# Kernel optimization log

Measured on AMD Instinct MI355X. Metric: run time of the kernel, lower is better.

## Reference

```python
import jax, jax.numpy as jnp
import numpy as np

# Hardcoded in FixedActionDecoder.__init__:
# action_words = [[click,submit,target,focus],[select,text,noun,username,password],[copy],[paste]]
ACTION_INDEX = jnp.array([0, 0, 0, 0, 1, 1, 1, 1, 1, 2, 3], dtype=jnp.int32)
POINT_SIZE = 11
ACTION_SIZE = 4
EPS = 1e-8  # F.cosine_similarity default eps


def setup_inputs() -> dict:
    key = jax.random.key(0)
    k1, k2 = jax.random.split(key)
    B, D = 1_000_000, 64
    return {
        "embedded_words": jax.random.normal(k1, (B, D), dtype=jnp.float32),
        "action_vectors": jax.random.normal(k2, (D, POINT_SIZE), dtype=jnp.float32),
    }


def reference(embedded_words, action_vectors):
    # Cosine similarity along the embedding dim (torch clamps each norm to eps).
    x = embedded_words / jnp.maximum(
        jnp.linalg.norm(embedded_words, axis=1, keepdims=True), EPS)          # [B, D]
    a = action_vectors / jnp.maximum(
        jnp.linalg.norm(action_vectors, axis=0, keepdims=True), EPS)          # [D, P]
    sims = x @ a                                                              # [B, P]
    # global_max_pool over batch_action_index == per-batch segment-max over actions.
    seg = jax.ops.segment_max(sims.T, ACTION_INDEX,
                              num_segments=ACTION_SIZE).T                     # [B, A]
    action_idx = jnp.argmax(seg, axis=1)                                      # [B]
    # one-hot scatter: ret[action_idx] = 1.0
    return jax.nn.one_hot(action_idx, ACTION_SIZE, dtype=embedded_words.dtype)
```

## Files before the change

kernel.cpp:

```cpp
#include <hip/hip_runtime.h>


#define NP 11
#define TAU 1e-3f
#define LROW 36
#define NROWS 128

__device__ __align__(16) float g_W32[704];
__device__ double g_W64[704];
__device__ unsigned long long g_bits[1 << 20];

__global__ void prep(const float* __restrict__ A) {
    int p = threadIdx.x;
    if (p < NP) {
        double ss = 0.0;
        for (int d = 0; d < 64; ++d) { double v = (double)A[d * NP + p]; ss += v * v; }
        double sc = 1.0 / fmax(sqrt(ss), 1e-8);
        for (int d = 0; d < 64; ++d) {
            double w = (double)A[d * NP + p] * sc;
            g_W64[d * NP + p] = w;
            g_W32[(d >> 2) * 44 + (d & 3) * NP + p] = (float)w;
        }
    }
}

__device__ __forceinline__ void argmax_gap(const float* s, int& idx, float& gap) {
    float m0 = fmaxf(fmaxf(s[0], s[1]), fmaxf(s[2], s[3]));
    float m1 = fmaxf(fmaxf(fmaxf(s[4], s[5]), s[6]), fmaxf(s[7], s[8]));
    float m2 = s[9], m3 = s[10];
    idx = 0; float best = m0;
    if (m1 > best) { best = m1; idx = 1; }
    if (m2 > best) { best = m2; idx = 2; }
    if (m3 > best) { best = m3; idx = 3; }
    float second = -3.4e38f;
    if (idx != 0) second = fmaxf(second, m0);
    if (idx != 1) second = fmaxf(second, m1);
    if (idx != 2) second = fmaxf(second, m2);
    if (idx != 3) second = fmaxf(second, m3);
    gap = best - second;
}

__global__ __launch_bounds__(128) void decode_f32(const float* __restrict__ X,
                                                  float* __restrict__ out, int B) {
    __shared__ float xbuf[2][NROWS][LROW];
    __shared__ float w_lds[704];

    const int tid = threadIdx.x;
    const int lane = tid & 63;
    const int wv = tid >> 6;
    float(*buf)[LROW] = xbuf[wv];

    for (int t = tid; t < 176; t += 128)
        reinterpret_cast<float4*>(w_lds)[t] =
            reinterpret_cast<const float4*>(g_W32)[t];
    __syncthreads();

    const float4* X4 = reinterpret_cast<const float4*>(X);
    const int gwave = blockIdx.x * 2 + wv;
    const int nwaves = gridDim.x * 2;

    #pragma unroll 1
    for (int base = gwave * NROWS; base < B; base += nwaves * NROWS) {
        float acc0[NP], acc1[NP];
        #pragma unroll
        for (int p = 0; p < NP; ++p) { acc0[p] = 0.0f; acc1[p] = 0.0f; }

        #pragma unroll
        for (int st = 0; st < 2; ++st) {
            #pragma unroll
            for (int i = 0; i < 16; ++i) {
                int fid = i * 64 + lane;
                int row = fid >> 3;
                int f = fid & 7;
                int r = base + row;
                if (r >= B) r = B - 1;
                float4 v = X4[(size_t)r * 16 + st * 8 + f];
                *reinterpret_cast<float4*>(&buf[row][f * 4]) = v;
            }
            __builtin_amdgcn_wave_barrier();

            #pragma unroll 1
            for (int kk = 0; kk < 8; ++kk) {
                const float* wrow = &w_lds[(st * 8 + kk) * 44];
                float4 x0 = *reinterpret_cast<const float4*>(&buf[lane][kk * 4]);
                float4 x1 = *reinterpret_cast<const float4*>(&buf[lane + 64][kk * 4]);
                #pragma unroll
                for (int p = 0; p < NP; ++p) {
                    float w0 = wrow[0 * NP + p], w1 = wrow[1 * NP + p];
                    float w2 = wrow[2 * NP + p], w3 = wrow[3 * NP + p];
                    float t0 = fmaf(x0.x, w0, acc0[p]);
                    t0 = fmaf(x0.y, w1, t0);
                    t0 = fmaf(x0.z, w2, t0);
                    acc0[p] = fmaf(x0.w, w3, t0);
                    float t1 = fmaf(x1.x, w0, acc1[p]);
                    t1 = fmaf(x1.y, w1, t1);
                    t1 = fmaf(x1.z, w2, t1);
                    acc1[p] = fmaf(x1.w, w3, t1);
                }
            }
            __builtin_amdgcn_wave_barrier();
        }

        int idx0, idx1; float gap0, gap1;
        argmax_gap(acc0, idx0, gap0);
        argmax_gap(acc1, idx1, gap1);

        unsigned long long m0 = __ballot(gap0 < TAU);
        unsigned long long m1 = __ballot(gap1 < TAU);
        if (lane == 0) {
            g_bits[(base >> 6) + 0] = m0;
            g_bits[(base >> 6) + 1] = m1;
        }

        int r0 = base + lane, r1 = base + 64 + lane;
        if (r0 < B) {
            float4 o;
            o.x = (idx0 == 0) ? 1.0f : 0.0f;
            o.y = (idx0 == 1) ? 1.0f : 0.0f;
            o.z = (idx0 == 2) ? 1.0f : 0.0f;
            o.w = (idx0 == 3) ? 1.0f : 0.0f;
            reinterpret_cast<float4*>(out)[r0] = o;
        }
        if (r1 < B) {
            float4 o;
            o.x = (idx1 == 0) ? 1.0f : 0.0f;
            o.y = (idx1 == 1) ? 1.0f : 0.0f;
            o.z = (idx1 == 2) ? 1.0f : 0.0f;
            o.w = (idx1 == 3) ? 1.0f : 0.0f;
            reinterpret_cast<float4*>(out)[r1] = o;
        }
    }
}

__global__ __launch_bounds__(256) void repair(const float* __restrict__ X,
                                              float* __restrict__ out, int B) {
    const int nwords = (B + 63) >> 6;
    for (int t = blockIdx.x * blockDim.x + threadIdx.x; t < nwords;
         t += gridDim.x * blockDim.x) {
        unsigned long long m = g_bits[t];
        while (m) {
            int b = __builtin_ctzll(m);
            m &= m - 1;
            int row = t * 64 + b;
            if (row >= B) continue;

            double s[NP];
            #pragma unroll
            for (int p = 0; p < NP; ++p) s[p] = 0.0;
            #pragma unroll 1
            for (int d = 0; d < 64; ++d) {
                double x = (double)X[(size_t)row * 64 + d];
                #pragma unroll
                for (int p = 0; p < NP; ++p)
                    s[p] = fma(x, g_W64[d * NP + p], s[p]);
            }

            double m0 = fmax(fmax(s[0], s[1]), fmax(s[2], s[3]));
            double m1 = fmax(fmax(fmax(s[4], s[5]), s[6]), fmax(s[7], s[8]));
            double m2 = s[9], m3 = s[10];
            int idx = 0; double best = m0;
            if (m1 > best) { best = m1; idx = 1; }
            if (m2 > best) { best = m2; idx = 2; }
            if (m3 > best) { best = m3; idx = 3; }

            float4 o;
            o.x = (idx == 0) ? 1.0f : 0.0f;
            o.y = (idx == 1) ? 1.0f : 0.0f;
            o.z = (idx == 2) ? 1.0f : 0.0f;
            o.w = (idx == 3) ? 1.0f : 0.0f;
            reinterpret_cast<float4*>(out)[row] = o;
        }
    }
}

extern "C" void kernel_launch(void* const* d_in, const int* in_sizes, int n_in,
                              void* d_out, int out_size, void* d_ws, size_t ws_size,
                              hipStream_t stream) {
    const float* X = (const float*)d_in[0];
    const float* A = (const float*)d_in[1];
    float* out = (float*)d_out;
    const int B = in_sizes[0] / 64;

    hipLaunchKernelGGL(prep, dim3(1), dim3(64), 0, stream, A);
    hipLaunchKernelGGL(decode_f32, dim3(1024), dim3(128), 0, stream, X, out, B);
    hipLaunchKernelGGL(repair, dim3(128), dim3(256), 0, stream, X, out, B);
}
```

Measured before the change: 88.64 us.

## Prefetch X tiles directly into LDS with double-buffered async global_load_lds

Each wave now streams its rows with global_load_lds straight into a swizzled LDS buffer for each half of the row, which skips the register staging step. The next tile's loads are issued right after the current half is consumed, so memory fetch overlaps with compute, and hand-placed vmcnt waits order the pipeline. Weights now live in the workspace and are read from global or constant memory instead of being staged in LDS, and the grid is halved to 512 blocks. This relies on fragile inline waitcnt counts and sched barriers. Per-wave LDS use also rises, which may limit occupancy.

Result: slower. 99.58 us (+12.3%).

```diff
diff --git a/kernel.cpp b/kernel.cpp
--- a/kernel.cpp
+++ b/kernel.cpp
@@ -3,14 +3,12 @@
 
 #define NP 11
 #define TAU 1e-3f
-#define LROW 36
-#define NROWS 128
-
-__device__ __align__(16) float g_W32[704];
-__device__ double g_W64[704];
+
 __device__ unsigned long long g_bits[1 << 20];
 
-__global__ void prep(const float* __restrict__ A) {
+__global__ void prep(const float* __restrict__ A, void* __restrict__ ws) {
+    float* W32 = (float*)ws;
+    double* W64 = (double*)((char*)ws + 4096);
     int p = threadIdx.x;
     if (p < NP) {
         double ss = 0.0;
@@ -18,11 +16,47 @@
         double sc = 1.0 / fmax(sqrt(ss), 1e-8);
         for (int d = 0; d < 64; ++d) {
             double w = (double)A[d * NP + p] * sc;
-            g_W64[d * NP + p] = w;
-            g_W32[(d >> 2) * 44 + (d & 3) * NP + p] = (float)w;
-        }
-    }
-}
+            W64[d * NP + p] = w;
+            W32[(d >> 2) * 44 + (d & 3) * NP + p] = (float)w;
+        }
+    }
+}
+
+#define ISSUE(tbase, phase, ldsbuf)                                            \
+    {                                                                          \
+        _Pragma("unroll") for (int i = 0; i < 16; ++i) {                       \
+            int row_local = i * 8 + (lane >> 3);                               \
+            int r = (tbase) + row_local;                                       \
+            if (r >= B) r = B - 1;     \
+            const float4* src = X4 + (size_t)r * 16 + (phase) * 8 + fsrc;      \
+            __builtin_amdgcn_global_load_lds(                                  \
+                (const __attribute__((address_space(1))) void*)src,            \
+                (__attribute__((address_space(3))) void*)((ldsbuf) + i * 64),  \
+                16, 0, 0);                                                     \
+        }                                                                      \
+    }
+
+#define COMPUTE(phase, buf)                                                    \
+    {                                                                          \
+        _Pragma("unroll 1") for (int kk = 0; kk < 8; ++kk) {                   \
+            const int sw = kk ^ s7;                                            \
+            float4 x0 = (buf)[lane * 8 + sw];                                  \
+            float4 x1 = (buf)[(lane + 64) * 8 + sw];                           \
+            const float* wrow = W + ((phase) * 8 + kk) * 44;                   \
+            _Pragma("unroll") for (int p = 0; p < NP; ++p) {                   \
+                float w0 = wrow[p], w1 = wrow[NP + p];                         \
+                float w2 = wrow[2 * NP + p], w3 = wrow[3 * NP + p];            \
+                float t0 = fmaf(x0.x, w0, acc0[p]);                            \
+                t0 = fmaf(x0.y, w1, t0);                                       \
+                t0 = fmaf(x0.z, w2, t0);                                       \
+                acc0[p] = fmaf(x0.w, w3, t0);                                  \
+                float t1 = fmaf(x1.x, w0, acc1[p]);                            \
+                t1 = fmaf(x1.y, w1, t1);                                       \
+                t1 = fmaf(x1.z, w2, t1);                                       \
+                acc1[p] = fmaf(x1.w, w3, t1);                                  \
+            }                                                                  \
+        }                                                                      \
+    }
 
 __device__ __forceinline__ void argmax_gap(const float* s, int& idx, float& gap) {
     float m0 = fmaxf(fmaxf(s[0], s[1]), fmaxf(s[2], s[3]));
@@ -40,66 +74,51 @@
     gap = best - second;
 }
 
-__global__ __launch_bounds__(128) void decode_f32(const float* __restrict__ X,
-                                                  float* __restrict__ out, int B) {
-    __shared__ float xbuf[2][NROWS][LROW];
-    __shared__ float w_lds[704];
+__global__ __launch_bounds__(128) void decode(const float* __restrict__ X,
+                                              float* __restrict__ out,
+                                              const float* __restrict__ W,
+                                              int B) {
+    __shared__ float4 sbuf[2][2][1024];
 
     const int tid = threadIdx.x;
     const int lane = tid & 63;
     const int wv = tid >> 6;
-    float(*buf)[LROW] = xbuf[wv];
-
-    for (int t = tid; t < 176; t += 128)
-        reinterpret_cast<float4*>(w_lds)[t] =
-            reinterpret_cast<const float4*>(g_W32)[t];
-    __syncthreads();
+    const int s7 = lane & 7;
+    const int fsrc = s7 ^ (lane >> 3);
+    float4* buf0 = &sbuf[wv][0][0];
+    float4* buf1 = &sbuf[wv][1][0];
 
     const float4* X4 = reinterpret_cast<const float4*>(X);
     const int gwave = blockIdx.x * 2 + wv;
-    const int nwaves = gridDim.x * 2;
+    const int stride = gridDim.x * 2 * 128;
+    const int base0 = gwave * 128;
+    if (base0 >= B) return;
+
+    ISSUE(base0, 0, buf0);
+    ISSUE(base0, 1, buf1);
 
     #pragma unroll 1
-    for (int base = gwave * NROWS; base < B; base += nwaves * NROWS) {
+    for (int base = base0; base < B; base += stride) {
+        const int next = base + stride;
+        const bool pf = next < B;
+
         float acc0[NP], acc1[NP];
         #pragma unroll
         for (int p = 0; p < NP; ++p) { acc0[p] = 0.0f; acc1[p] = 0.0f; }
 
-        #pragma unroll
-        for (int st = 0; st < 2; ++st) {
-            #pragma unroll
-            for (int i = 0; i < 16; ++i) {
-                int fid = i * 64 + lane;
-                int row = fid >> 3;
-                int f = fid & 7;
-                int r = base + row;
-                if (r >= B) r = B - 1;
-                float4 v = X4[(size_t)r * 16 + st * 8 + f];
-                *reinterpret_cast<float4*>(&buf[row][f * 4]) = v;
-            }
-            __builtin_amdgcn_wave_barrier();
-
-            #pragma unroll 1
-            for (int kk = 0; kk < 8; ++kk) {
-                const float* wrow = &w_lds[(st * 8 + kk) * 44];
-                float4 x0 = *reinterpret_cast<const float4*>(&buf[lane][kk * 4]);
-                float4 x1 = *reinterpret_cast<const float4*>(&buf[lane + 64][kk * 4]);
-                #pragma unroll
-                for (int p = 0; p < NP; ++p) {
-                    float w0 = wrow[0 * NP + p], w1 = wrow[1 * NP + p];
-                    float w2 = wrow[2 * NP + p], w3 = wrow[3 * NP + p];
-                    float t0 = fmaf(x0.x, w0, acc0[p]);
-                    t0 = fmaf(x0.y, w1, t0);
-                    t0 = fmaf(x0.z, w2, t0);
-                    acc0[p] = fmaf(x0.w, w3, t0);
-                    float t1 = fmaf(x1.x, w0, acc1[p]);
-                    t1 = fmaf(x1.y, w1, t1);
-                    t1 = fmaf(x1.z, w2, t1);
-                    acc1[p] = fmaf(x1.w, w3, t1);
-                }
-            }
-            __builtin_amdgcn_wave_barrier();
-        }
+        asm volatile("s_waitcnt vmcnt(16)" ::: "memory");
+        __builtin_amdgcn_sched_barrier(0);
+        COMPUTE(0, buf0);
+        if (pf) ISSUE(next, 0, buf0);
+
+        if (pf) {
+            asm volatile("s_waitcnt vmcnt(16)" ::: "memory");
+        } else {
+            asm volatile("s_waitcnt vmcnt(0)" ::: "memory");
+        }
+        __builtin_amdgcn_sched_barrier(0);
+        COMPUTE(1, buf1);
+        if (pf) ISSUE(next, 1, buf1);
 
         int idx0, idx1; float gap0, gap1;
         argmax_gap(acc0, idx0, gap0);
@@ -133,7 +152,10 @@
 }
 
 __global__ __launch_bounds__(256) void repair(const float* __restrict__ X,
-                                              float* __restrict__ out, int B) {
+                                              float* __restrict__ out,
+                                              const void* __restrict__ ws,
+                                              int B) {
+    const double* W64 = (const double*)((const char*)ws + 4096);
     const int nwords = (B + 63) >> 6;
     for (int t = blockIdx.x * blockDim.x + threadIdx.x; t < nwords;
          t += gridDim.x * blockDim.x) {
@@ -152,7 +174,7 @@
                 double x = (double)X[(size_t)row * 64 + d];
                 #pragma unroll
                 for (int p = 0; p < NP; ++p)
-                    s[p] = fma(x, g_W64[d * NP + p], s[p]);
+                    s[p] = fma(x, W64[d * NP + p], s[p]);
             }
 
             double m0 = fmax(fmax(s[0], s[1]), fmax(s[2], s[3]));
@@ -181,7 +203,8 @@
     float* out = (float*)d_out;
     const int B = in_sizes[0] / 64;
 
-    hipLaunchKernelGGL(prep, dim3(1), dim3(64), 0, stream, A);
-    hipLaunchKernelGGL(decode_f32, dim3(1024), dim3(128), 0, stream, X, out, B);
-    hipLaunchKernelGGL(repair, dim3(128), dim3(256), 0, stream, X, out, B);
-}
+    hipLaunchKernelGGL(prep, dim3(1), dim3(64), 0, stream, A, d_ws);
+    hipLaunchKernelGGL(decode, dim3(512), dim3(128), 0, stream,
+                       X, out, (const float*)d_ws, B);
+    hipLaunchKernelGGL(repair, dim3(128), dim3(256), 0, stream, X, out, d_ws, B);
+}
```

## Software-pipeline X loads through registers with 256-row wave tiles

Applied to the files above, without the earlier changes.

Each wave now handles 256 rows, split into four 16-float column quarters. The next quarter's global loads are issued into registers while the current quarter is computed out of LDS, so global memory latency overlaps with the FMA work. Each lane holds four rows of accumulators, which raises register pressure. The grid shrinks to 768 blocks and the LDS row pitch drops to 20 floats, which can change bank conflicts.

Result: slower. 201.0 us (+126.8%).

```diff
diff --git a/kernel.cpp b/kernel.cpp
--- a/kernel.cpp
+++ b/kernel.cpp
@@ -3,8 +3,7 @@
 
 #define NP 11
 #define TAU 1e-3f
-#define LROW 36
-#define NROWS 128
+#define QS 20
 
 __device__ __align__(16) float g_W32[704];
 __device__ double g_W64[704];
@@ -40,15 +39,15 @@
     gap = best - second;
 }
 
-__global__ __launch_bounds__(128) void decode_f32(const float* __restrict__ X,
-                                                  float* __restrict__ out, int B) {
-    __shared__ float xbuf[2][NROWS][LROW];
+__global__ __launch_bounds__(128) void decode(const float* __restrict__ X,
+                                              float* __restrict__ out, int B) {
+    __shared__ float xq[2][256][QS];
     __shared__ float w_lds[704];
 
     const int tid = threadIdx.x;
     const int lane = tid & 63;
     const int wv = tid >> 6;
-    float(*buf)[LROW] = xbuf[wv];
+    float(*buf)[QS] = xq[wv];
 
     for (int t = tid; t < 176; t += 128)
         reinterpret_cast<float4*>(w_lds)[t] =
@@ -57,77 +56,93 @@
 
     const float4* X4 = reinterpret_cast<const float4*>(X);
     const int gwave = blockIdx.x * 2 + wv;
-    const int nwaves = gridDim.x * 2;
+    const int stride = gridDim.x * 2 * 256;
+    const int base0 = gwave * 256;
+    if (base0 >= B) return;
+
+    const int srow = lane >> 2;
+    const int sf = lane & 3;
+
+    float4 st[16];
+
+    #pragma unroll
+    for (int i = 0; i < 16; ++i) {
+        int r = base0 + i * 16 + srow;
+        if (r >= B) r = B - 1;
+        st[i] = X4[(size_t)r * 16 + sf];
+    }
 
     #pragma unroll 1
-    for (int base = gwave * NROWS; base < B; base += nwaves * NROWS) {
-        float acc0[NP], acc1[NP];
+    for (int base = base0; base < B; base += stride) {
+        const int next = base + stride;
+
+        float acc[4][NP];
         #pragma unroll
-        for (int p = 0; p < NP; ++p) { acc0[p] = 0.0f; acc1[p] = 0.0f; }
-
-        #pragma unroll
-        for (int st = 0; st < 2; ++st) {
+        for (int j = 0; j < 4; ++j)
             #pragma unroll
-            for (int i = 0; i < 16; ++i) {
-                int fid = i * 64 + lane;
-                int row = fid >> 3;
-                int f = fid & 7;
-                int r = base + row;
-                if (r >= B) r = B - 1;
-                float4 v = X4[(size_t)r * 16 + st * 8 + f];
-                *reinterpret_cast<float4*>(&buf[row][f * 4]) = v;
-            }
+            for (int p = 0; p < NP; ++p) acc[j][p] = 0.0f;
+
+        #pragma unroll 1
+        for (int q = 0; q < 4; ++q) {
+            asm volatile("s_waitcnt vmcnt(0)" ::: "memory");
+            __builtin_amdgcn_sched_barrier(0);
+            #pragma unroll
+            for (int i = 0; i < 16; ++i)
+                *reinterpret_cast<float4*>(&buf[i * 16 + srow][sf * 4]) = st[i];
             __builtin_amdgcn_wave_barrier();
+            __builtin_amdgcn_sched_barrier(0);
+
+            int nq = q + 1, nbase = base;
+            if (nq == 4) { nq = 0; nbase = next; }
+            if (nbase < B) {
+                #pragma unroll
+                for (int i = 0; i < 16; ++i) {
+                    int r = nbase + i * 16 + srow;
+                    if (r >= B) r = B - 1;
+                    st[i] = X4[(size_t)r * 16 + nq * 4 + sf];
+                }
+            }
 
             #pragma unroll 1
-            for (int kk = 0; kk < 8; ++kk) {
-                const float* wrow = &w_lds[(st * 8 + kk) * 44];
+            for (int kk = 0; kk < 4; ++kk) {
+                const float* wrow = &w_lds[(q * 4 + kk) * 44];
                 float4 x0 = *reinterpret_cast<const float4*>(&buf[lane][kk * 4]);
                 float4 x1 = *reinterpret_cast<const float4*>(&buf[lane + 64][kk * 4]);
+                float4 x2 = *reinterpret_cast<const float4*>(&buf[lane + 128][kk * 4]);
+                float4 x3 = *reinterpret_cast<const float4*>(&buf[lane + 192][kk * 4]);
                 #pragma unroll
                 for (int p = 0; p < NP; ++p) {
-                    float w0 = wrow[0 * NP + p], w1 = wrow[1 * NP + p];
+                    float w0 = wrow[p], w1 = wrow[NP + p];
                     float w2 = wrow[2 * NP + p], w3 = wrow[3 * NP + p];
-                    float t0 = fmaf(x0.x, w0, acc0[p]);
-                    t0 = fmaf(x0.y, w1, t0);
-                    t0 = fmaf(x0.z, w2, t0);
-                    acc0[p] = fmaf(x0.w, w3, t0);
-                    float t1 = fmaf(x1.x, w0, acc1[p]);
-                    t1 = fmaf(x1.y, w1, t1);
-                    t1 = fmaf(x1.z, w2, t1);
-                    acc1[p] = fmaf(x1.w, w3, t1);
+                    float t;
+                    t = fmaf(x0.x, w0, acc[0][p]); t = fmaf(x0.y, w1, t);
+                    t = fmaf(x0.z, w2, t);         acc[0][p] = fmaf(x0.w, w3, t);
+                    t = fmaf(x1.x, w0, acc[1][p]); t = fmaf(x1.y, w1, t);
+                    t = fmaf(x1.z, w2, t);         acc[1][p] = fmaf(x1.w, w3, t);
+                    t = fmaf(x2.x, w0, acc[2][p]); t = fmaf(x2.y, w1, t);
+                    t = fmaf(x2.z, w2, t);         acc[2][p] = fmaf(x2.w, w3, t);
+                    t = fmaf(x3.x, w0, acc[3][p]); t = fmaf(x3.y, w1, t);
+                    t = fmaf(x3.z, w2, t);         acc[3][p] = fmaf(x3.w, w3, t);
                 }
             }
             __builtin_amdgcn_wave_barrier();
         }
 
-        int idx0, idx1; float gap0, gap1;
-        argmax_gap(acc0, idx0, gap0);
-        argmax_gap(acc1, idx1, gap1);
-
-        unsigned long long m0 = __ballot(gap0 < TAU);
-        unsigned long long m1 = __ballot(gap1 < TAU);
-        if (lane == 0) {
-            g_bits[(base >> 6) + 0] = m0;
-            g_bits[(base >> 6) + 1] = m1;
-        }
-
-        int r0 = base + lane, r1 = base + 64 + lane;
-        if (r0 < B) {
-            float4 o;
-            o.x = (idx0 == 0) ? 1.0f : 0.0f;
-            o.y = (idx0 == 1) ? 1.0f : 0.0f;
-            o.z = (idx0 == 2) ? 1.0f : 0.0f;
-            o.w = (idx0 == 3) ? 1.0f : 0.0f;
-            reinterpret_cast<float4*>(out)[r0] = o;
-        }
-        if (r1 < B) {
-            float4 o;
-            o.x = (idx1 == 0) ? 1.0f : 0.0f;
-            o.y = (idx1 == 1) ? 1.0f : 0.0f;
-            o.z = (idx1 == 2) ? 1.0f : 0.0f;
-            o.w = (idx1 == 3) ? 1.0f : 0.0f;
-            reinterpret_cast<float4*>(out)[r1] = o;
+        #pragma unroll
+        for (int j = 0; j < 4; ++j) {
+            int idx; float gap;
+            argmax_gap(acc[j], idx, gap);
+            unsigned long long m = __ballot(gap < TAU);
+            if (lane == 0) g_bits[(base >> 6) + j] = m;
+            int r = base + j * 64 + lane;
+            if (r < B) {
+                float4 o;
+                o.x = (idx == 0) ? 1.0f : 0.0f;
+                o.y = (idx == 1) ? 1.0f : 0.0f;
+                o.z = (idx == 2) ? 1.0f : 0.0f;
+                o.w = (idx == 3) ? 1.0f : 0.0f;
+                reinterpret_cast<float4*>(out)[r] = o;
+            }
         }
     }
 }
@@ -182,6 +197,6 @@
     const int B = in_sizes[0] / 64;
 
     hipLaunchKernelGGL(prep, dim3(1), dim3(64), 0, stream, A);
-    hipLaunchKernelGGL(decode_f32, dim3(1024), dim3(128), 0, stream, X, out, B);
+    hipLaunchKernelGGL(decode, dim3(768), dim3(128), 0, stream, X, out, B);
     hipLaunchKernelGGL(repair, dim3(128), dim3(256), 0, stream, X, out, B);
 }
```

## Transpose weight layout for float4 LDS loads, parallelize prep, cache weights in repair

Applied to the files above, without the earlier changes.

The normalized weight table is now stored so that the four k-values for each action point sit next to each other. The decode inner loop can then fetch them with one float4 LDS read instead of four scalar reads. The prep kernel now uses all 64 threads, with a shared-memory reduction, instead of 11 serial threads. The repair kernel stages the double-precision weights in LDS rather than reading global memory on every FMA. The aim is to cut LDS instruction count in the hot loop and to shorten the serial prep and repair phases.

Result: faster. 78.28 us (median of 3 runs) (-11.7%).

```diff
diff --git a/kernel.cpp b/kernel.cpp
--- a/kernel.cpp
+++ b/kernel.cpp
@@ -4,23 +4,34 @@
 #define NP 11
 #define TAU 1e-3f
 #define LROW 36
-#define NROWS 128
 
 __device__ __align__(16) float g_W32[704];
 __device__ double g_W64[704];
 __device__ unsigned long long g_bits[1 << 20];
 
 __global__ void prep(const float* __restrict__ A) {
-    int p = threadIdx.x;
-    if (p < NP) {
+    __shared__ double sq[64][NP + 1];
+    __shared__ double sc[NP];
+    const int d = threadIdx.x;
+    double a[NP];
+    #pragma unroll
+    for (int p = 0; p < NP; ++p) {
+        a[p] = (double)A[d * NP + p];
+        sq[d][p] = a[p] * a[p];
+    }
+    __syncthreads();
+    if (d < NP) {
         double ss = 0.0;
-        for (int d = 0; d < 64; ++d) { double v = (double)A[d * NP + p]; ss += v * v; }
-        double sc = 1.0 / fmax(sqrt(ss), 1e-8);
-        for (int d = 0; d < 64; ++d) {
-            double w = (double)A[d * NP + p] * sc;
-            g_W64[d * NP + p] = w;
-            g_W32[(d >> 2) * 44 + (d & 3) * NP + p] = (float)w;
-        }
+        #pragma unroll
+        for (int r = 0; r < 64; ++r) ss += sq[r][d];
+        sc[d] = 1.0 / fmax(sqrt(ss), 1e-8);
+    }
+    __syncthreads();
+    #pragma unroll
+    for (int p = 0; p < NP; ++p) {
+        double w = a[p] * sc[p];
+        g_W64[d * NP + p] = w;
+        g_W32[(d >> 2) * 44 + p * 4 + (d & 3)] = (float)w;
     }
 }
 
@@ -40,9 +51,9 @@
     gap = best - second;
 }
 
-__global__ __launch_bounds__(128) void decode_f32(const float* __restrict__ X,
-                                                  float* __restrict__ out, int B) {
-    __shared__ float xbuf[2][NROWS][LROW];
+__global__ __launch_bounds__(128) void decode(const float* __restrict__ X,
+                                              float* __restrict__ out, int B) {
+    __shared__ float xbuf[2][128][LROW];
     __shared__ float w_lds[704];
 
     const int tid = threadIdx.x;
@@ -60,7 +71,7 @@
     const int nwaves = gridDim.x * 2;
 
     #pragma unroll 1
-    for (int base = gwave * NROWS; base < B; base += nwaves * NROWS) {
+    for (int base = gwave * 128; base < B; base += nwaves * 128) {
         float acc0[NP], acc1[NP];
         #pragma unroll
         for (int p = 0; p < NP; ++p) { acc0[p] = 0.0f; acc1[p] = 0.0f; }
@@ -86,16 +97,15 @@
                 float4 x1 = *reinterpret_cast<const float4*>(&buf[lane + 64][kk * 4]);
                 #pragma unroll
                 for (int p = 0; p < NP; ++p) {
-                    float w0 = wrow[0 * NP + p], w1 = wrow[1 * NP + p];
-                    float w2 = wrow[2 * NP + p], w3 = wrow[3 * NP + p];
-                    float t0 = fmaf(x0.x, w0, acc0[p]);
-                    t0 = fmaf(x0.y, w1, t0);
-                    t0 = fmaf(x0.z, w2, t0);
-                    acc0[p] = fmaf(x0.w, w3, t0);
-                    float t1 = fmaf(x1.x, w0, acc1[p]);
-                    t1 = fmaf(x1.y, w1, t1);
-                    t1 = fmaf(x1.z, w2, t1);
-                    acc1[p] = fmaf(x1.w, w3, t1);
+                    float4 wq = *reinterpret_cast<const float4*>(&wrow[p * 4]);
+                    float t0 = fmaf(x0.x, wq.x, acc0[p]);
+                    t0 = fmaf(x0.y, wq.y, t0);
+                    t0 = fmaf(x0.z, wq.z, t0);
+                    acc0[p] = fmaf(x0.w, wq.w, t0);
+                    float t1 = fmaf(x1.x, wq.x, acc1[p]);
+                    t1 = fmaf(x1.y, wq.y, t1);
+                    t1 = fmaf(x1.z, wq.z, t1);
+                    acc1[p] = fmaf(x1.w, wq.w, t1);
                 }
             }
             __builtin_amdgcn_wave_barrier();
@@ -134,8 +144,13 @@
 
 __global__ __launch_bounds__(256) void repair(const float* __restrict__ X,
                                               float* __restrict__ out, int B) {
+    __shared__ double w64[704];
+    const int tid = threadIdx.x;
+    for (int i = tid; i < 704; i += 256) w64[i] = g_W64[i];
+    __syncthreads();
+
     const int nwords = (B + 63) >> 6;
-    for (int t = blockIdx.x * blockDim.x + threadIdx.x; t < nwords;
+    for (int t = blockIdx.x * blockDim.x + tid; t < nwords;
          t += gridDim.x * blockDim.x) {
         unsigned long long m = g_bits[t];
         while (m) {
@@ -152,7 +167,7 @@
                 double x = (double)X[(size_t)row * 64 + d];
                 #pragma unroll
                 for (int p = 0; p < NP; ++p)
-                    s[p] = fma(x, g_W64[d * NP + p], s[p]);
+                    s[p] = fma(x, w64[d * NP + p], s[p]);
             }
 
             double m0 = fmax(fmax(s[0], s[1]), fmax(s[2], s[3]));
@@ -182,6 +197,6 @@
     const int B = in_sizes[0] / 64;
 
     hipLaunchKernelGGL(prep, dim3(1), dim3(64), 0, stream, A);
-    hipLaunchKernelGGL(decode_f32, dim3(1024), dim3(128), 0, stream, X, out, B);
+    hipLaunchKernelGGL(decode, dim3(1024), dim3(128), 0, stream, X, out, B);
     hipLaunchKernelGGL(repair, dim3(128), dim3(256), 0, stream, X, out, B);
 }
```
